# Kernel optimization log

Measured on AMD Instinct MI355X. Metric: run time of the kernel, lower is better.

The kernel has to match this reference:

```python
import jax, jax.numpy as jnp
import numpy as np

B, T_ENC, T_DEC = 8, 1024, 100
DMODEL, H, DK, DV, DFF = 512, 8, 64, 64, 2048
L_ENC, L_DEC = 2, 2
EPS = 1e-5
MASK_FILL = -1e10  # original code masked_fills the post-softmax probs with -1e10


def _ln(x, g, b):
    m = jnp.mean(x, -1, keepdims=True)
    v = jnp.mean(jnp.square(x - m), -1, keepdims=True)
    return (x - m) * jax.lax.rsqrt(v + EPS) * g + b


def _mha(Q, K, V, Wq, Wk, Wv, causal):
    Bz, Lq, _ = Q.shape
    Lk = K.shape[1]
    q = (Q @ Wq).reshape(Bz, Lq, H, DK).transpose(0, 2, 1, 3)  # b h q d
    k = (K @ Wk).reshape(Bz, Lk, H, DK).transpose(0, 2, 1, 3)
    v = (V @ Wv).reshape(Bz, Lk, H, DV).transpose(0, 2, 1, 3)
    scores = jnp.einsum('bhqd,bhkd->bhqk', q, k) * (1.0 / np.float32(np.sqrt(DK)))
    p = jax.nn.softmax(scores, axis=-1)
    if causal:
        # faithful to original: mask applied AFTER softmax, fill value -1e10
        mask = jnp.tril(jnp.ones((Lq, Lk), dtype=bool))
        p = jnp.where(mask[None, None], p, jnp.float32(MASK_FILL))
    o = jnp.einsum('bhqk,bhkd->bhqd', p, v)
    return o.transpose(0, 2, 1, 3).reshape(Bz, Lq, H * DV)


def setup_inputs() -> dict:
    key = jax.random.key(0)
    ks = iter(jax.random.split(key, 64))
    s = 0.02
    d = {
        'x': jax.random.normal(next(ks), (B, T_ENC, DMODEL), jnp.float32),
        'y': jax.random.normal(next(ks), (B, T_DEC, DMODEL), jnp.float32),
    }
    def w(shape):
        return jax.random.normal(next(ks), shape, jnp.float32) * s
    # encoder params, stacked over layers
    d['enc_Wq'] = w((L_ENC, DMODEL, DMODEL)); d['enc_Wk'] = w((L_ENC, DMODEL, H * DK))
    d['enc_Wv'] = w((L_ENC, DMODEL, H * DV))
    d['enc_ff_w1'] = w((L_ENC, DMODEL, DFF)); d['enc_ff_b1'] = jnp.zeros((L_ENC, DFF))
    d['enc_ff_w2'] = w((L_ENC, DFF, DMODEL)); d['enc_ff_b2'] = jnp.zeros((L_ENC, DMODEL))
    d['enc_ln1_g'] = jnp.ones((L_ENC, DMODEL)); d['enc_ln1_b'] = jnp.zeros((L_ENC, DMODEL))
    d['enc_ln2_g'] = jnp.ones((L_ENC, DMODEL)); d['enc_ln2_b'] = jnp.zeros((L_ENC, DMODEL))
    # decoder params
    d['dec_Wq1'] = w((L_DEC, DMODEL, DMODEL)); d['dec_Wk1'] = w((L_DEC, DMODEL, H * DK))
    d['dec_Wv1'] = w((L_DEC, DMODEL, H * DV))
    d['dec_Wq2'] = w((L_DEC, DMODEL, DMODEL)); d['dec_Wk2'] = w((L_DEC, DMODEL, H * DK))
    d['dec_Wv2'] = w((L_DEC, DMODEL, H * DV))
    d['dec_ff_w1'] = w((L_DEC, DMODEL, DFF)); d['dec_ff_b1'] = jnp.zeros((L_DEC, DFF))
    d['dec_ff_w2'] = w((L_DEC, DFF, DMODEL)); d['dec_ff_b2'] = jnp.zeros((L_DEC, DMODEL))
    d['dec_ln1_g'] = jnp.ones((L_DEC, DMODEL)); d['dec_ln1_b'] = jnp.zeros((L_DEC, DMODEL))
    d['dec_ln2_g'] = jnp.ones((L_DEC, DMODEL)); d['dec_ln2_b'] = jnp.zeros((L_DEC, DMODEL))
    d['dec_ln3_g'] = jnp.ones((L_DEC, DMODEL)); d['dec_ln3_b'] = jnp.zeros((L_DEC, DMODEL))
    return d


def reference(x, y,
              enc_Wq, enc_Wk, enc_Wv, enc_ff_w1, enc_ff_b1, enc_ff_w2, enc_ff_b2,
              enc_ln1_g, enc_ln1_b, enc_ln2_g, enc_ln2_b,
              dec_Wq1, dec_Wk1, dec_Wv1, dec_Wq2, dec_Wk2, dec_Wv2,
              dec_ff_w1, dec_ff_b1, dec_ff_w2, dec_ff_b2,
              dec_ln1_g, dec_ln1_b, dec_ln2_g, dec_ln2_b, dec_ln3_g, dec_ln3_b):
    # encoder stacks
    for i in range(L_ENC):
        att = _mha(x, x, x, enc_Wq[i], enc_Wk[i], enc_Wv[i], causal=False)
        x1 = _ln(x + att, enc_ln1_g[i], enc_ln1_b[i])
        ff = jax.nn.relu(x1 @ enc_ff_w1[i] + enc_ff_b1[i]) @ enc_ff_w2[i] + enc_ff_b2[i]
        x = _ln(x1 + ff, enc_ln2_g[i], enc_ln2_b[i])
    # decoder stacks
    for i in range(L_DEC):
        a1 = _mha(y, y, y, dec_Wq1[i], dec_Wk1[i], dec_Wv1[i], causal=True)
        y1 = _ln(y + a1, dec_ln1_g[i], dec_ln1_b[i])
        a2 = _mha(y1, x, x, dec_Wq2[i], dec_Wk2[i], dec_Wv2[i], causal=False)
        y2 = _ln(y1 + a2, dec_ln2_g[i], dec_ln2_b[i])
        ff = jax.nn.relu(y2 @ dec_ff_w1[i] + dec_ff_b1[i]) @ dec_ff_w2[i] + dec_ff_b2[i]
        y = _ln(y2 + ff, dec_ln3_g[i], dec_ln3_b[i])
    return y
```

## Files before the change

### kernel.cpp

```cpp
#include <hip/hip_runtime.h>
#include <cstddef>

typedef unsigned short u16;
typedef __attribute__((ext_vector_type(8))) short bf16x8;
typedef __attribute__((ext_vector_type(4))) float f32x4;

__device__ __forceinline__ u16 f2b(float f) {
    union { float f; unsigned u; } x; x.f = f;
    unsigned r = x.u + 0x7FFFu + ((x.u >> 16) & 1u);
    return (u16)(r >> 16);
}
__device__ __forceinline__ float b2f(u16 v) {
    union { unsigned u; float f; } x; x.u = ((unsigned)v) << 16;
    return x.f;
}

__device__ __forceinline__ void gload_lds16(const u16* g, u16* l) {
    __builtin_amdgcn_global_load_lds(
        (const __attribute__((address_space(1))) void*)g,
        (__attribute__((address_space(3))) void*)l, 16, 0, 0);
}

__global__ __launch_bounds__(256) void gemm_mfma_kernel(
    const u16* __restrict__ A, const u16* __restrict__ Bt,
    const float* __restrict__ bias,
    float* __restrict__ Cf, u16* __restrict__ Cb,
    int M, int K, int N, int relu)
{
    __shared__ __align__(16) u16 As[128 * 64];
    __shared__ __align__(16) u16 Bs[128 * 64];

    const int tid  = threadIdx.x;
    const int wave = tid >> 6;
    const int lane = tid & 63;
    const int m0 = blockIdx.y * 128;
    const int n0 = blockIdx.x * 128;

    const int wm = (wave & 1) * 64;
    const int wn = (wave >> 1) * 64;

    const int srow  = lane >> 3;
    const int skoff = (lane & 7) * 8;

    f32x4 acc[4][4];
#pragma unroll
    for (int i = 0; i < 4; ++i)
#pragma unroll
        for (int j = 0; j < 4; ++j)
            acc[i][j] = (f32x4){0.f, 0.f, 0.f, 0.f};

    const int fm = lane & 15;
    const int fq = (lane >> 4) * 8;

    for (int k0 = 0; k0 < K; k0 += 64) {
        __syncthreads();
        {
            const int r0 = wave * 32;
#pragma unroll
            for (int t = 0; t < 4; ++t) {
                int gr = m0 + r0 + t * 8 + srow; if (gr >= M) gr = M - 1;
                gload_lds16(A + (size_t)gr * K + k0 + skoff, &As[(r0 + t * 8) * 64]);
                gload_lds16(Bt + (size_t)(n0 + r0 + t * 8 + srow) * K + k0 + skoff,
                            &Bs[(r0 + t * 8) * 64]);
            }
        }
        __syncthreads();

#pragma unroll
        for (int kk = 0; kk < 64; kk += 32) {
            bf16x8 af[4], bfr[4];
#pragma unroll
            for (int t = 0; t < 4; ++t) {
                af[t]  = *(const bf16x8*)(&As[(wm + t * 16 + fm) * 64 + fq + kk]);
                bfr[t] = *(const bf16x8*)(&Bs[(wn + t * 16 + fm) * 64 + fq + kk]);
            }
#pragma unroll
            for (int i = 0; i < 4; ++i)
#pragma unroll
                for (int j = 0; j < 4; ++j)
                    acc[i][j] = __builtin_amdgcn_mfma_f32_16x16x32_bf16(
                        af[i], bfr[j], acc[i][j], 0, 0, 0);
        }
    }

    const int col = lane & 15;
    const int rq  = (lane >> 4) * 4;
#pragma unroll
    for (int j = 0; j < 4; ++j) {
        const int gn = n0 + wn + j * 16 + col;
        const float bb = bias ? bias[gn] : 0.f;
#pragma unroll
        for (int i = 0; i < 4; ++i) {
            const int gmb = m0 + wm + i * 16 + rq;
#pragma unroll
            for (int r = 0; r < 4; ++r) {
                const int gm = gmb + r;
                if (gm < M) {
                    float v = acc[i][j][r] + bb;
                    if (relu) v = fmaxf(v, 0.f);
                    if (Cb) Cb[(size_t)gm * N + gn] = f2b(v);
                    else    Cf[(size_t)gm * N + gn] = v;
                }
            }
        }
    }
}

__global__ __launch_bounds__(256) void gemm64_kernel(
    const u16* __restrict__ A, const u16* __restrict__ Bt,
    const float* __restrict__ bias,
    float* __restrict__ Cf, u16* __restrict__ Cb,
    int M, int K, int N, int relu)
{
    __shared__ __align__(16) u16 As[64 * 64];
    __shared__ __align__(16) u16 Bs[64 * 64];

    const int tid  = threadIdx.x;
    const int wave = tid >> 6;
    const int lane = tid & 63;
    const int m0 = blockIdx.y * 64;
    const int n0 = blockIdx.x * 64;
    const int wm = (wave & 1) * 32;
    const int wn = (wave >> 1) * 32;

    const int srow  = lane >> 3;
    const int skoff = (lane & 7) * 8;

    f32x4 acc[2][2];
#pragma unroll
    for (int i = 0; i < 2; ++i)
#pragma unroll
        for (int j = 0; j < 2; ++j) acc[i][j] = (f32x4){0.f, 0.f, 0.f, 0.f};

    const int fm = lane & 15;
    const int fq = (lane >> 4) * 8;

    for (int k0 = 0; k0 < K; k0 += 64) {
        __syncthreads();
        {
#pragma unroll
            for (int t = 0; t < 2; ++t) {
                int gr = m0 + t * 32 + wave * 8 + srow; if (gr >= M) gr = M - 1;
                gload_lds16(A + (size_t)gr * K + k0 + skoff, &As[(t * 32 + wave * 8) * 64]);
                gload_lds16(Bt + (size_t)(n0 + t * 32 + wave * 8 + srow) * K + k0 + skoff,
                            &Bs[(t * 32 + wave * 8) * 64]);
            }
        }
        __syncthreads();

#pragma unroll
        for (int kk = 0; kk < 64; kk += 32) {
            bf16x8 af[2], bfr[2];
#pragma unroll
            for (int t = 0; t < 2; ++t) {
                af[t]  = *(const bf16x8*)(&As[(wm + t * 16 + fm) * 64 + fq + kk]);
                bfr[t] = *(const bf16x8*)(&Bs[(wn + t * 16 + fm) * 64 + fq + kk]);
            }
#pragma unroll
            for (int i = 0; i < 2; ++i)
#pragma unroll
                for (int j = 0; j < 2; ++j)
                    acc[i][j] = __builtin_amdgcn_mfma_f32_16x16x32_bf16(
                        af[i], bfr[j], acc[i][j], 0, 0, 0);
        }
    }

    const int col = lane & 15;
    const int rq  = (lane >> 4) * 4;
#pragma unroll
    for (int j = 0; j < 2; ++j) {
        const int gn = n0 + wn + j * 16 + col;
        const float bb = bias ? bias[gn] : 0.f;
#pragma unroll
        for (int i = 0; i < 2; ++i) {
            const int gmb = m0 + wm + i * 16 + rq;
#pragma unroll
            for (int r = 0; r < 4; ++r) {
                const int gm = gmb + r;
                if (gm < M) {
                    float v = acc[i][j][r] + bb;
                    if (relu) v = fmaxf(v, 0.f);
                    if (Cb) Cb[(size_t)gm * N + gn] = f2b(v);
                    else    Cf[(size_t)gm * N + gn] = v;
                }
            }
        }
    }
}

__global__ __launch_bounds__(256) void attn_mfma_kernel(
    const u16* __restrict__ Qp, const u16* __restrict__ Kp,
    const u16* __restrict__ Vp, u16* __restrict__ Op,
    int Lq, int Lk, int ldq, int ldkv, int ldo)
{
    const int q0 = blockIdx.x * 128;
    const int h  = blockIdx.y;
    const int b  = blockIdx.z;
    const int tid  = threadIdx.x;
    const int wave = tid >> 6;
    const int lane = tid & 63;
    const int c = lane & 15;
    const int g = lane >> 4;
    const float scale = 0.125f;

    __shared__ __align__(16) u16 Ks[128 * 72];
    __shared__ __align__(16) u16 Vs[64 * 144];
    __shared__ __align__(16) u16 Ps[128 * 144];

    bf16x8 aq[2][2];
#pragma unroll
    for (int half = 0; half < 2; ++half) {
        int qrow = q0 + wave * 32 + half * 16 + c;
        if (qrow > Lq - 1) qrow = Lq - 1;
        const u16* src = Qp + ((size_t)(b * Lq + qrow)) * ldq + h * 64 + g * 8;
        aq[half][0] = *(const bf16x8*)(src);
        aq[half][1] = *(const bf16x8*)(src + 32);
    }

    float den[2][4] = {};
    f32x4 o[2][4];
#pragma unroll
    for (int half = 0; half < 2; ++half)
#pragma unroll
        for (int j = 0; j < 4; ++j) o[half][j] = (f32x4){0.f, 0.f, 0.f, 0.f};

    const int srow = tid & 63;
    const int sseg = tid >> 6;

    for (int t = 0; t < (Lk >> 7); ++t) {
        const int k0 = t << 7;
        __syncthreads();
#pragma unroll
        for (int sub = 0; sub < 2; ++sub) {
            const int kr = k0 + sub * 64 + srow;
            const u16* kg = Kp + ((size_t)(b * Lk + kr)) * ldkv + h * 64;
            *(bf16x8*)(&Ks[(sub * 64 + srow) * 72 + sseg * 8])      = *(const bf16x8*)(kg + sseg * 8);
            *(bf16x8*)(&Ks[(sub * 64 + srow) * 72 + 32 + sseg * 8]) = *(const bf16x8*)(kg + 32 + sseg * 8);
            const u16* vg = Vp + ((size_t)(b * Lk + kr)) * ldkv + h * 64;
            bf16x8 v0 = *(const bf16x8*)(vg + sseg * 8);
            bf16x8 v1 = *(const bf16x8*)(vg + 32 + sseg * 8);
#pragma unroll
            for (int i = 0; i < 8; ++i) {
                Vs[(sseg * 8 + i) * 144 + sub * 64 + srow]      = (u16)v0[i];
                Vs[(32 + sseg * 8 + i) * 144 + sub * 64 + srow] = (u16)v1[i];
            }
        }
        __syncthreads();

#pragma unroll
        for (int half = 0; half < 2; ++half) {
            f32x4 s[8];
#pragma unroll
            for (int jn = 0; jn < 8; ++jn) s[jn] = (f32x4){0.f, 0.f, 0.f, 0.f};
#pragma unroll
            for (int jn = 0; jn < 8; ++jn) {
                bf16x8 b0 = *(const bf16x8*)(&Ks[(jn * 16 + c) * 72 + g * 8]);
                bf16x8 b1 = *(const bf16x8*)(&Ks[(jn * 16 + c) * 72 + 32 + g * 8]);
                s[jn] = __builtin_amdgcn_mfma_f32_16x16x32_bf16(aq[half][0], b0, s[jn], 0, 0, 0);
                s[jn] = __builtin_amdgcn_mfma_f32_16x16x32_bf16(aq[half][1], b1, s[jn], 0, 0, 0);
            }
#pragma unroll
            for (int jn = 0; jn < 8; ++jn)
#pragma unroll
                for (int r = 0; r < 4; ++r) {
                    const float p = __expf(s[jn][r] * scale);
                    den[half][r] += p;
                    Ps[(wave * 32 + half * 16 + g * 4 + r) * 144 + jn * 16 + c] = f2b(p);
                }
        }

        __asm__ volatile("s_waitcnt lgkmcnt(0)" ::: "memory");

#pragma unroll
        for (int half = 0; half < 2; ++half) {
            const int qr = (wave * 32 + half * 16 + c) * 144;
#pragma unroll
            for (int sub = 0; sub < 2; ++sub) {
                bf16x8 ap0 = *(const bf16x8*)(&Ps[qr + sub * 64 + g * 8]);
                bf16x8 ap1 = *(const bf16x8*)(&Ps[qr + sub * 64 + 32 + g * 8]);
#pragma unroll
                for (int jd = 0; jd < 4; ++jd) {
                    bf16x8 b0 = *(const bf16x8*)(&Vs[(jd * 16 + c) * 144 + sub * 64 + g * 8]);
                    bf16x8 b1 = *(const bf16x8*)(&Vs[(jd * 16 + c) * 144 + sub * 64 + 32 + g * 8]);
                    o[half][jd] = __builtin_amdgcn_mfma_f32_16x16x32_bf16(ap0, b0, o[half][jd], 0, 0, 0);
                    o[half][jd] = __builtin_amdgcn_mfma_f32_16x16x32_bf16(ap1, b1, o[half][jd], 0, 0, 0);
                }
            }
        }
    }

#pragma unroll
    for (int half = 0; half < 2; ++half)
#pragma unroll
        for (int r = 0; r < 4; ++r) {
#pragma unroll
            for (int msk = 1; msk < 16; msk <<= 1)
                den[half][r] += __shfl_xor(den[half][r], msk, 64);
        }

#pragma unroll
    for (int half = 0; half < 2; ++half)
#pragma unroll
        for (int r = 0; r < 4; ++r) {
            const int q = q0 + wave * 32 + half * 16 + g * 4 + r;
            if (q < Lq) {
                const float inv = 1.0f / den[half][r];
#pragma unroll
                for (int jd = 0; jd < 4; ++jd)
                    Op[((size_t)(b * Lq + q)) * ldo + h * 64 + jd * 16 + c] =
                        f2b(o[half][jd][r] * inv);
            }
        }
}

__global__ __launch_bounds__(256) void attn_causal_kernel(
    const u16* __restrict__ Qp, const u16* __restrict__ Kp,
    const u16* __restrict__ Vp, const float* __restrict__ SuffV,
    u16* __restrict__ Op,
    int Lq, int Lk, int ldq, int ldkv, int ldo)
{
    const int q0 = blockIdx.x * 128;
    const int h  = blockIdx.y;
    const int b  = blockIdx.z;
    const int tid  = threadIdx.x;
    const int wave = tid >> 6;
    const int lane = tid & 63;
    const int c = lane & 15;
    const int g = lane >> 4;
    const float scale = 0.125f;

    __shared__ __align__(16) u16 Ks[64 * 72];
    __shared__ __align__(16) u16 Vs[64 * 72];
    __shared__ __align__(16) u16 Ps[128 * 72];

    bf16x8 aq[2][2];
#pragma unroll
    for (int half = 0; half < 2; ++half) {
        int qrow = q0 + wave * 32 + half * 16 + c;
        if (qrow > Lq - 1) qrow = Lq - 1;
        const u16* src = Qp + ((size_t)(b * Lq + qrow)) * ldq + h * 64 + g * 8;
        aq[half][0] = *(const bf16x8*)(src);
        aq[half][1] = *(const bf16x8*)(src + 32);
    }

    float den[2][4] = {};
    f32x4 o[2][4];
#pragma unroll
    for (int half = 0; half < 2; ++half)
#pragma unroll
        for (int j = 0; j < 4; ++j) o[half][j] = (f32x4){0.f, 0.f, 0.f, 0.f};

    const int srow = tid & 63;
    const int sseg = tid >> 6;
    const int ntiles = (Lk + 63) >> 6;

    for (int t = 0; t < ntiles; ++t) {
        const int k0 = t << 6;
        __syncthreads();
        {
            int kr = k0 + srow; if (kr > Lk - 1) kr = Lk - 1;
            const u16* kg = Kp + ((size_t)(b * Lk + kr)) * ldkv + h * 64;
            *(bf16x8*)(&Ks[srow * 72 + sseg * 8])      = *(const bf16x8*)(kg + sseg * 8);
            *(bf16x8*)(&Ks[srow * 72 + 32 + sseg * 8]) = *(const bf16x8*)(kg + 32 + sseg * 8);
            const u16* vg = Vp + ((size_t)(b * Lk + kr)) * ldkv + h * 64;
            bf16x8 v0 = *(const bf16x8*)(vg + sseg * 8);
            bf16x8 v1 = *(const bf16x8*)(vg + 32 + sseg * 8);
#pragma unroll
            for (int i = 0; i < 8; ++i) {
                Vs[(sseg * 8 + i) * 72 + srow]      = (u16)v0[i];
                Vs[(32 + sseg * 8 + i) * 72 + srow] = (u16)v1[i];
            }
        }
        __syncthreads();

#pragma unroll
        for (int half = 0; half < 2; ++half) {
            f32x4 s[4];
#pragma unroll
            for (int jn = 0; jn < 4; ++jn) s[jn] = (f32x4){0.f, 0.f, 0.f, 0.f};
#pragma unroll
            for (int jn = 0; jn < 4; ++jn) {
                bf16x8 b0 = *(const bf16x8*)(&Ks[(jn * 16 + c) * 72 + g * 8]);
                bf16x8 b1 = *(const bf16x8*)(&Ks[(jn * 16 + c) * 72 + 32 + g * 8]);
                s[jn] = __builtin_amdgcn_mfma_f32_16x16x32_bf16(aq[half][0], b0, s[jn], 0, 0, 0);
                s[jn] = __builtin_amdgcn_mfma_f32_16x16x32_bf16(aq[half][1], b1, s[jn], 0, 0, 0);
            }
#pragma unroll
            for (int jn = 0; jn < 4; ++jn)
#pragma unroll
                for (int r = 0; r < 4; ++r) {
                    const int kcol = k0 + jn * 16 + c;
                    const int qrow = q0 + wave * 32 + half * 16 + g * 4 + r;
                    const float e = __expf(s[jn][r] * scale);
                    const float ev = (kcol < Lk) ? e : 0.f;
                    den[half][r] += ev;
                    const float pv = (kcol <= qrow) ? ev : 0.f;
                    Ps[(wave * 32 + half * 16 + g * 4 + r) * 72 + jn * 16 + c] = f2b(pv);
                }
        }

        __asm__ volatile("s_waitcnt lgkmcnt(0)" ::: "memory");

#pragma unroll
        for (int half = 0; half < 2; ++half) {
            bf16x8 ap0 = *(const bf16x8*)(&Ps[(wave * 32 + half * 16 + c) * 72 + g * 8]);
            bf16x8 ap1 = *(const bf16x8*)(&Ps[(wave * 32 + half * 16 + c) * 72 + 32 + g * 8]);
#pragma unroll
            for (int jd = 0; jd < 4; ++jd) {
                bf16x8 b0 = *(const bf16x8*)(&Vs[(jd * 16 + c) * 72 + g * 8]);
                bf16x8 b1 = *(const bf16x8*)(&Vs[(jd * 16 + c) * 72 + 32 + g * 8]);
                o[half][jd] = __builtin_amdgcn_mfma_f32_16x16x32_bf16(ap0, b0, o[half][jd], 0, 0, 0);
                o[half][jd] = __builtin_amdgcn_mfma_f32_16x16x32_bf16(ap1, b1, o[half][jd], 0, 0, 0);
            }
        }
    }

#pragma unroll
    for (int half = 0; half < 2; ++half)
#pragma unroll
        for (int r = 0; r < 4; ++r) {
#pragma unroll
            for (int msk = 1; msk < 16; msk <<= 1)
                den[half][r] += __shfl_xor(den[half][r], msk, 64);
        }

#pragma unroll
    for (int half = 0; half < 2; ++half)
#pragma unroll
        for (int r = 0; r < 4; ++r) {
            const int q = q0 + wave * 32 + half * 16 + g * 4 + r;
            if (q < Lq) {
                const float inv = 1.0f / den[half][r];
                const float* sv = SuffV + ((size_t)(b * Lq + q)) * 512 + h * 64;
#pragma unroll
                for (int jd = 0; jd < 4; ++jd)
                    Op[((size_t)(b * Lq + q)) * ldo + h * 64 + jd * 16 + c] =
                        f2b(o[half][jd][r] * inv - 1.0e10f * sv[jd * 16 + c]);
            }
        }
}

__global__ __launch_bounds__(64) void suffv_kernel(
    const u16* __restrict__ Vp, float* __restrict__ SuffV, int Lq, int ldv)
{
    const int b = blockIdx.x;
    const int h = blockIdx.y;
    const int d = threadIdx.x;
    float acc = 0.f;
    for (int q = Lq - 1; q >= 0; --q) {
        SuffV[((size_t)(b * Lq + q)) * 512 + h * 64 + d] = acc;
        acc += b2f(Vp[((size_t)(b * Lq + q)) * ldv + h * 64 + d]);
    }
}

__global__ __launch_bounds__(256) void attn_split_kernel(
    const u16* __restrict__ Qp, const u16* __restrict__ Kp,
    const u16* __restrict__ Vp, float* __restrict__ Opart,
    float* __restrict__ Dpart,
    int Lq, int Lk, int ldq, int ldkv, int nsplit)
{
    const int q0 = blockIdx.x * 64;
    const int h  = blockIdx.y;
    const int b  = blockIdx.z / nsplit;
    const int sp = blockIdx.z % nsplit;
    const int tid  = threadIdx.x;
    const int wave = tid >> 6;
    const int lane = tid & 63;
    const int c = lane & 15;
    const int g = lane >> 4;
    const float scale = 0.125f;
    const int rowsTot = gridDim.z / nsplit * Lq;

    __shared__ __align__(16) u16 Ks[64 * 72];
    __shared__ __align__(16) u16 Vs[64 * 72];
    __shared__ __align__(16) u16 Ps[64 * 72];

    bf16x8 aq[2];
    {
        int qrow = q0 + wave * 16 + c;
        if (qrow > Lq - 1) qrow = Lq - 1;
        const u16* src = Qp + ((size_t)(b * Lq + qrow)) * ldq + h * 64 + g * 8;
        aq[0] = *(const bf16x8*)(src);
        aq[1] = *(const bf16x8*)(src + 32);
    }

    float den[4] = {0.f, 0.f, 0.f, 0.f};
    f32x4 o[4];
#pragma unroll
    for (int j = 0; j < 4; ++j) o[j] = (f32x4){0.f, 0.f, 0.f, 0.f};

    const int srow = tid & 63;
    const int sseg = tid >> 6;
    const int ntile = (Lk >> 6) / nsplit;

    for (int t = sp * ntile; t < (sp + 1) * ntile; ++t) {
        const int k0 = t << 6;
        __syncthreads();
        {
            const u16* kg = Kp + ((size_t)(b * Lk + k0 + srow)) * ldkv + h * 64;
            *(bf16x8*)(&Ks[srow * 72 + sseg * 8])      = *(const bf16x8*)(kg + sseg * 8);
            *(bf16x8*)(&Ks[srow * 72 + 32 + sseg * 8]) = *(const bf16x8*)(kg + 32 + sseg * 8);
            const u16* vg = Vp + ((size_t)(b * Lk + k0 + srow)) * ldkv + h * 64;
            bf16x8 v0 = *(const bf16x8*)(vg + sseg * 8);
            bf16x8 v1 = *(const bf16x8*)(vg + 32 + sseg * 8);
#pragma unroll
            for (int i = 0; i < 8; ++i) {
                Vs[(sseg * 8 + i) * 72 + srow]      = (u16)v0[i];
                Vs[(32 + sseg * 8 + i) * 72 + srow] = (u16)v1[i];
            }
        }
        __syncthreads();

        f32x4 s[4];
#pragma unroll
        for (int jn = 0; jn < 4; ++jn) s[jn] = (f32x4){0.f, 0.f, 0.f, 0.f};
#pragma unroll
        for (int jn = 0; jn < 4; ++jn) {
            bf16x8 b0 = *(const bf16x8*)(&Ks[(jn * 16 + c) * 72 + g * 8]);
            bf16x8 b1 = *(const bf16x8*)(&Ks[(jn * 16 + c) * 72 + 32 + g * 8]);
            s[jn] = __builtin_amdgcn_mfma_f32_16x16x32_bf16(aq[0], b0, s[jn], 0, 0, 0);
            s[jn] = __builtin_amdgcn_mfma_f32_16x16x32_bf16(aq[1], b1, s[jn], 0, 0, 0);
        }
#pragma unroll
        for (int jn = 0; jn < 4; ++jn)
#pragma unroll
            for (int r = 0; r < 4; ++r) {
                const float p = __expf(s[jn][r] * scale);
                den[r] += p;
                Ps[(wave * 16 + g * 4 + r) * 72 + jn * 16 + c] = f2b(p);
            }

        __asm__ volatile("s_waitcnt lgkmcnt(0)" ::: "memory");

        bf16x8 ap0 = *(const bf16x8*)(&Ps[(wave * 16 + c) * 72 + g * 8]);
        bf16x8 ap1 = *(const bf16x8*)(&Ps[(wave * 16 + c) * 72 + 32 + g * 8]);
#pragma unroll
        for (int jd = 0; jd < 4; ++jd) {
            bf16x8 b0 = *(const bf16x8*)(&Vs[(jd * 16 + c) * 72 + g * 8]);
            bf16x8 b1 = *(const bf16x8*)(&Vs[(jd * 16 + c) * 72 + 32 + g * 8]);
            o[jd] = __builtin_amdgcn_mfma_f32_16x16x32_bf16(ap0, b0, o[jd], 0, 0, 0);
            o[jd] = __builtin_amdgcn_mfma_f32_16x16x32_bf16(ap1, b1, o[jd], 0, 0, 0);
        }
    }

#pragma unroll
    for (int r = 0; r < 4; ++r) {
#pragma unroll
        for (int msk = 1; msk < 16; msk <<= 1)
            den[r] += __shfl_xor(den[r], msk, 64);
    }

#pragma unroll
    for (int r = 0; r < 4; ++r) {
        const int q = q0 + wave * 16 + g * 4 + r;
        if (q < Lq) {
            const size_t prow = (size_t)sp * rowsTot + b * Lq + q;
#pragma unroll
            for (int jd = 0; jd < 4; ++jd)
                Opart[prow * 512 + h * 64 + jd * 16 + c] = o[jd][r];
            if (c == 0) Dpart[prow * 8 + h] = den[r];
        }
    }
}

__global__ __launch_bounds__(256) void combine_ln_kernel(
    const float* __restrict__ Opart, const float* __restrict__ Dpart,
    int nsplit, int nrows,
    const float* __restrict__ R,
    const float* __restrict__ g, const float* __restrict__ beta,
    float* __restrict__ O, u16* __restrict__ Ob)
{
    const int row = blockIdx.x * 4 + (threadIdx.x >> 6);
    const int lane = threadIdx.x & 63;
    if (row >= nrows) return;
    const size_t base = (size_t)row * 512 + lane * 8;
    const int h = lane >> 3;

    float sd = 0.f;
    float v[8] = {};
    for (int s = 0; s < nsplit; ++s) {
        sd += Dpart[((size_t)s * nrows + row) * 8 + h];
        const float* op = Opart + ((size_t)s * nrows + row) * 512 + lane * 8;
        float4 a = *(const float4*)(op);
        float4 b = *(const float4*)(op + 4);
        v[0] += a.x; v[1] += a.y; v[2] += a.z; v[3] += a.w;
        v[4] += b.x; v[5] += b.y; v[6] += b.z; v[7] += b.w;
    }
    const float invd = 1.0f / sd;
    {
        float4 a = *(const float4*)(R + base);
        float4 b = *(const float4*)(R + base + 4);
        v[0] = v[0] * invd + a.x; v[1] = v[1] * invd + a.y;
        v[2] = v[2] * invd + a.z; v[3] = v[3] * invd + a.w;
        v[4] = v[4] * invd + b.x; v[5] = v[5] * invd + b.y;
        v[6] = v[6] * invd + b.z; v[7] = v[7] * invd + b.w;
    }

    float sum = 0.f;
#pragma unroll
    for (int i = 0; i < 8; ++i) sum += v[i];
#pragma unroll
    for (int msk = 1; msk < 64; msk <<= 1) sum += __shfl_xor(sum, msk, 64);
    const float mean = sum * (1.0f / 512.0f);

    float var = 0.f;
#pragma unroll
    for (int i = 0; i < 8; ++i) { v[i] -= mean; var += v[i] * v[i]; }
#pragma unroll
    for (int msk = 1; msk < 64; msk <<= 1) var += __shfl_xor(var, msk, 64);
    const float rstd = rsqrtf(var * (1.0f / 512.0f) + 1e-5f);

    float o[8];
#pragma unroll
    for (int i = 0; i < 8; ++i)
        o[i] = v[i] * rstd * g[lane * 8 + i] + beta[lane * 8 + i];

    *(float4*)(O + base)     = make_float4(o[0], o[1], o[2], o[3]);
    *(float4*)(O + base + 4) = make_float4(o[4], o[5], o[6], o[7]);
    if (Ob) {
        bf16x8 ob;
#pragma unroll
        for (int i = 0; i < 8; ++i) ob[i] = (short)f2b(o[i]);
        *(bf16x8*)(Ob + base) = ob;
    }
}

struct WT9 { const float* src[9]; unsigned dst[9]; unsigned os[9]; };
struct WT4 { const float* src[4]; unsigned dst[4]; int K[4]; int N[4]; };

__device__ __forceinline__ void wtrans_tile(
    const float* Wl, u16* Wtl, int K, int N, int k0, int n0, int tid)
{
    __shared__ float t[32][33];
    const int tr = tid >> 3;
    const int tc = (tid & 7) * 4;
    float4 v = *(const float4*)(Wl + (size_t)(k0 + tr) * N + n0 + tc);
    t[tr][tc] = v.x; t[tr][tc + 1] = v.y; t[tr][tc + 2] = v.z; t[tr][tc + 3] = v.w;
    __syncthreads();
    ushort4 o;
    o.x = f2b(t[tc + 0][tr]); o.y = f2b(t[tc + 1][tr]);
    o.z = f2b(t[tc + 2][tr]); o.w = f2b(t[tc + 3][tr]);
    *(ushort4*)(Wtl + (size_t)(n0 + tr) * K + k0 + tc) = o;
}

__global__ __launch_bounds__(256) void wtrans9_kernel(WT9 d, u16* __restrict__ WB)
{
    const int w = blockIdx.z >> 1;
    const int layer = blockIdx.z & 1;
    const float* Wl = d.src[w] + (size_t)layer * 512 * 512;
    u16* Wtl = WB + d.dst[w] + (size_t)layer * d.os[w];
    wtrans_tile(Wl, Wtl, 512, 512, blockIdx.y * 32, blockIdx.x * 32, threadIdx.x);
}

__global__ __launch_bounds__(256) void wtrans4_kernel(WT4 d, u16* __restrict__ WB)
{
    const int w = blockIdx.z >> 1;
    const int layer = blockIdx.z & 1;
    const int K = d.K[w], N = d.N[w];
    const int k0 = blockIdx.y * 32, n0 = blockIdx.x * 32;
    if (k0 >= K || n0 >= N) return;
    const float* Wl = d.src[w] + (size_t)layer * K * N;
    u16* Wtl = WB + d.dst[w] + (size_t)layer * 1048576;
    wtrans_tile(Wl, Wtl, K, N, k0, n0, threadIdx.x);
}

__global__ __launch_bounds__(256) void conv2_kernel(
    const float* __restrict__ X0, u16* __restrict__ Y0, int n0,
    const float* __restrict__ X1, u16* __restrict__ Y1, int n1)
{
    int i = (blockIdx.x * 256 + threadIdx.x) * 8;
    const float* X; u16* Y;
    if (i < n0) { X = X0 + i; Y = Y0 + i; }
    else if (i < n0 + n1) { X = X1 + (i - n0); Y = Y1 + (i - n0); }
    else return;
    float4 a = *(const float4*)(X);
    float4 b = *(const float4*)(X + 4);
    ushort4 o0, o1;
    o0.x = f2b(a.x); o0.y = f2b(a.y); o0.z = f2b(a.z); o0.w = f2b(a.w);
    o1.x = f2b(b.x); o1.y = f2b(b.y); o1.z = f2b(b.z); o1.w = f2b(b.w);
    *(ushort4*)(Y) = o0;
    *(ushort4*)(Y + 4) = o1;
}

__global__ __launch_bounds__(256) void ln_kernel(
    const float* __restrict__ Xf, const u16* __restrict__ Xb,
    const float* __restrict__ R,
    const float* __restrict__ g, const float* __restrict__ beta,
    float* __restrict__ O, u16* __restrict__ Ob, int nrows)
{
    const int row = blockIdx.x * 4 + (threadIdx.x >> 6);
    const int lane = threadIdx.x & 63;
    if (row >= nrows) return;
    const size_t base = (size_t)row * 512 + lane * 8;

    float v[8];
    if (Xf) {
        float4 a = *(const float4*)(Xf + base);
        float4 b = *(const float4*)(Xf + base + 4);
        v[0] = a.x; v[1] = a.y; v[2] = a.z; v[3] = a.w;
        v[4] = b.x; v[5] = b.y; v[6] = b.z; v[7] = b.w;
    } else {
        bf16x8 xb = *(const bf16x8*)(Xb + base);
#pragma unroll
        for (int i = 0; i < 8; ++i) v[i] = b2f((u16)xb[i]);
    }
    {
        float4 a = *(const float4*)(R + base);
        float4 b = *(const float4*)(R + base + 4);
        v[0] += a.x; v[1] += a.y; v[2] += a.z; v[3] += a.w;
        v[4] += b.x; v[5] += b.y; v[6] += b.z; v[7] += b.w;
    }

    float sum = 0.f;
#pragma unroll
    for (int i = 0; i < 8; ++i) sum += v[i];
#pragma unroll
    for (int msk = 1; msk < 64; msk <<= 1) sum += __shfl_xor(sum, msk, 64);
    const float mean = sum * (1.0f / 512.0f);

    float var = 0.f;
#pragma unroll
    for (int i = 0; i < 8; ++i) { v[i] -= mean; var += v[i] * v[i]; }
#pragma unroll
    for (int msk = 1; msk < 64; msk <<= 1) var += __shfl_xor(var, msk, 64);
    const float rstd = rsqrtf(var * (1.0f / 512.0f) + 1e-5f);

    float o[8];
#pragma unroll
    for (int i = 0; i < 8; ++i)
        o[i] = v[i] * rstd * g[lane * 8 + i] + beta[lane * 8 + i];

    *(float4*)(O + base)     = make_float4(o[0], o[1], o[2], o[3]);
    *(float4*)(O + base + 4) = make_float4(o[4], o[5], o[6], o[7]);
    if (Ob) {
        bf16x8 ob;
#pragma unroll
        for (int i = 0; i < 8; ++i) ob[i] = (short)f2b(o[i]);
        *(bf16x8*)(Ob + base) = ob;
    }
}

extern "C" void kernel_launch(void* const* d_in, const int* in_sizes, int n_in,
                              void* d_out, int out_size, void* d_ws, size_t ws_size,
                              hipStream_t stream)
{
    const int B = 8, T_ENC = 1024, T_DEC = 100, DM = 512, DFF = 2048;
    const int ME = B * T_ENC;
    const int MD = B * T_DEC;
    const int L = 2;
    const int NSPLIT = 4;

    int idx = 0;
    const float* x0    = (const float*)d_in[idx++];
    const float* y0    = (const float*)d_in[idx++];
    const float* eWq   = (const float*)d_in[idx++];
    const float* eWk   = (const float*)d_in[idx++];
    const float* eWv   = (const float*)d_in[idx++];
    const float* eW1   = (const float*)d_in[idx++];
    const float* eB1   = (const float*)d_in[idx++];
    const float* eW2   = (const float*)d_in[idx++];
    const float* eB2   = (const float*)d_in[idx++];
    const float* eLn1g = (const float*)d_in[idx++];
    const float* eLn1b = (const float*)d_in[idx++];
    const float* eLn2g = (const float*)d_in[idx++];
    const float* eLn2b = (const float*)d_in[idx++];
    const float* dWq1  = (const float*)d_in[idx++];
    const float* dWk1  = (const float*)d_in[idx++];
    const float* dWv1  = (const float*)d_in[idx++];
    const float* dWq2  = (const float*)d_in[idx++];
    const float* dWk2  = (const float*)d_in[idx++];
    const float* dWv2  = (const float*)d_in[idx++];
    const float* dW1   = (const float*)d_in[idx++];
    const float* dB1   = (const float*)d_in[idx++];
    const float* dW2   = (const float*)d_in[idx++];
    const float* dB2   = (const float*)d_in[idx++];
    const float* dLn1g = (const float*)d_in[idx++];
    const float* dLn1b = (const float*)d_in[idx++];
    const float* dLn2g = (const float*)d_in[idx++];
    const float* dLn2b = (const float*)d_in[idx++];
    const float* dLn3g = (const float*)d_in[idx++];
    const float* dLn3b = (const float*)d_in[idx++];

    float* ws = (float*)d_ws;
    u16* OV    = (u16*)ws;
    u16* QKVb  = OV;
    u16* H1b   = OV;
    u16* CKVb  = OV;
    u16* AFb    = (u16*)(ws + 8388608);
    float* Dpart = ws + 8388608;
    float* X1   = ws + 10485760;
    float* XOUT = ws + 14680064;
    float* SuffV = ws + 18874368;
    float* Opart = ws + 18874368;
    float* DA    = ws + 20103168;
    float* Y1   = ws + 20512768;
    float* Y2   = ws + 20922368;
    float* YOUT = ws + 21331968;
    u16* ub  = (u16*)(ws + 21741568);
    u16* XBc = ub;
    u16* YB  = ub + 4194304;
    u16* Y1b = ub + 4603904;
    u16* Y2b = ub + 5013504;
    u16* DQb = ub + 5423104;
    u16* DAb = ub + 5832704;
    u16* DHb = ub + 6242304;
    u16* DQKVb = DHb;
    u16* WB  = ub + 7880704;

    const unsigned eQKVT = 0, eW1T = 1572864, eW2T = 3670016,
                   dQKV1T = 5767168, dWq2T = 7340032, dKV2T = 7864320,
                   dW1T = 8912896, dW2T = 11010048;

    auto gemm = [&](const u16* A, const u16* Bt, const float* bias, float* Cf, u16* Cb,
                    int M, int K, int N, int relu) {
        dim3 grid(N / 128, (M + 127) / 128);
        hipLaunchKernelGGL(gemm_mfma_kernel, grid, dim3(256), 0, stream,
                           A, Bt, bias, Cf, Cb, M, K, N, relu);
    };
    auto gemm64 = [&](const u16* A, const u16* Bt, const float* bias, float* Cf, u16* Cb,
                      int M, int K, int N, int relu) {
        dim3 grid(N / 64, (M + 63) / 64);
        hipLaunchKernelGGL(gemm64_kernel, grid, dim3(256), 0, stream,
                           A, Bt, bias, Cf, Cb, M, K, N, relu);
    };
    auto ln = [&](const float* Xf, const u16* Xb, const float* R, const float* g,
                  const float* bta, float* O, u16* Ob, int rows) {
        hipLaunchKernelGGL(ln_kernel, dim3((rows + 3) / 4), dim3(256), 0, stream,
                           Xf, Xb, R, g, bta, O, Ob, rows);
    };

    {
        WT9 w9;
        const float* s9[9] = {eWq, eWk, eWv, dWq1, dWk1, dWv1, dWq2, dWk2, dWv2};
        const unsigned d9[9] = {eQKVT, eQKVT + 262144, eQKVT + 524288,
                                dQKV1T, dQKV1T + 262144, dQKV1T + 524288,
                                dWq2T, dKV2T, dKV2T + 262144};
        const unsigned o9[9] = {786432, 786432, 786432, 786432, 786432, 786432,
                                262144, 524288, 524288};
        for (int i = 0; i < 9; ++i) { w9.src[i] = s9[i]; w9.dst[i] = d9[i]; w9.os[i] = o9[i]; }
        hipLaunchKernelGGL(wtrans9_kernel, dim3(16, 16, 18), dim3(256), 0, stream, w9, WB);

        WT4 w4;
        const float* s4[4] = {eW1, eW2, dW1, dW2};
        const unsigned d4[4] = {eW1T, eW2T, dW1T, dW2T};
        const int K4[4] = {512, 2048, 512, 2048};
        const int N4[4] = {2048, 512, 2048, 512};
        for (int i = 0; i < 4; ++i) { w4.src[i] = s4[i]; w4.dst[i] = d4[i]; w4.K[i] = K4[i]; w4.N[i] = N4[i]; }
        hipLaunchKernelGGL(wtrans4_kernel, dim3(64, 64, 8), dim3(256), 0, stream, w4, WB);

        const int n0 = ME * DM, n1 = MD * DM;
        hipLaunchKernelGGL(conv2_kernel, dim3((n0 + n1) / 8 / 256), dim3(256), 0, stream,
                           x0, XBc, n0, y0, YB, n1);
    }

    const int BS = DM;
    const int B1S = DFF;

    const float* xin = x0;
    for (int i = 0; i < L; ++i) {
        gemm(XBc, WB + eQKVT + (size_t)i * 786432, nullptr, nullptr, QKVb, ME, DM, 1536, 0);
        {
            dim3 grid(T_ENC / 128, 8, B);
            hipLaunchKernelGGL(attn_mfma_kernel, grid, dim3(256), 0, stream,
                               QKVb, QKVb + 512, QKVb + 1024, AFb,
                               T_ENC, T_ENC, 1536, 1536, 512);
        }
        ln(nullptr, AFb, xin, eLn1g + i * BS, eLn1b + i * BS, X1, XBc, ME);
        gemm(XBc, WB + eW1T + (size_t)i * 1048576, eB1 + i * B1S, nullptr, H1b, ME, DM, DFF, 1);
        gemm(H1b, WB + eW2T + (size_t)i * 1048576, eB2 + i * BS, nullptr, AFb, ME, DFF, DM, 0);
        ln(nullptr, AFb, X1, eLn2g + i * BS, eLn2b + i * BS, XOUT, XBc, ME);
        xin = XOUT;
    }

    gemm(XBc, WB + dKV2T, nullptr, nullptr, CKVb, ME, DM, 2048, 0);

    const float* yin = y0;
    for (int i = 0; i < L; ++i) {
        gemm64(YB, WB + dQKV1T + (size_t)i * 786432, nullptr, nullptr, DQKVb, MD, DM, 1536, 0);
        hipLaunchKernelGGL(suffv_kernel, dim3(B, 8), dim3(64), 0, stream,
                           DQKVb + 1024, SuffV, T_DEC, 1536);
        {
            dim3 grid((T_DEC + 127) / 128, 8, B);
            hipLaunchKernelGGL(attn_causal_kernel, grid, dim3(256), 0, stream,
                               DQKVb, DQKVb + 512, DQKVb + 1024, SuffV, DAb,
                               T_DEC, T_DEC, 1536, 1536, 512);
        }
        ln(nullptr, DAb, yin, dLn1g + i * BS, dLn1b + i * BS, Y1, Y1b, MD);
        gemm64(Y1b, WB + dWq2T + (size_t)i * 262144, nullptr, nullptr, DQb, MD, DM, DM, 0);
        {
            dim3 grid((T_DEC + 63) / 64, 8, B * NSPLIT);
            hipLaunchKernelGGL(attn_split_kernel, grid, dim3(256), 0, stream,
                               DQb, CKVb + (size_t)i * 1024, CKVb + (size_t)i * 1024 + 512,
                               Opart, Dpart, T_DEC, T_ENC, 512, 2048, NSPLIT);
            hipLaunchKernelGGL(combine_ln_kernel, dim3((MD + 3) / 4), dim3(256), 0, stream,
                               Opart, Dpart, NSPLIT, MD,
                               Y1, dLn2g + i * BS, dLn2b + i * BS, Y2, Y2b);
        }
        gemm64(Y2b, WB + dW1T + (size_t)i * 1048576, dB1 + i * B1S, nullptr, DHb, MD, DM, DFF, 1);
        gemm64(DHb, WB + dW2T + (size_t)i * 1048576, dB2 + i * BS, DA, nullptr, MD, DFF, DM, 0);
        float* yout = (i == L - 1) ? (float*)d_out : YOUT;
        ln(DA, nullptr, Y2, dLn3g + i * BS, dLn3b + i * BS, yout,
           (i == L - 1) ? nullptr : YB, MD);
        yin = yout;
    }
}
```

Measured before the change: 863.1 us.

## Double-buffer LDS tiles in MFMA GEMM kernels with K-step of 32

Both GEMM kernels now keep two LDS buffers with a K-tile of 32 instead of a single 64-wide buffer. The next tile's global-to-LDS load is issued before the current tile's MFMAs run, using manual vmcnt/lgkmcnt waits and raw barriers in place of __syncthreads. The goal is to hide global load latency behind compute. In exchange there are twice as many loop iterations and barriers per K, and correctness depends on the hand-tuned waitcnt counts.

```diff
diff --git a/kernel.cpp b/kernel.cpp
--- a/kernel.cpp
+++ b/kernel.cpp
@@ -27,8 +27,8 @@
     float* __restrict__ Cf, u16* __restrict__ Cb,
     int M, int K, int N, int relu)
 {
-    __shared__ __align__(16) u16 As[128 * 64];
-    __shared__ __align__(16) u16 Bs[128 * 64];
+    __shared__ __align__(16) u16 As[2][128 * 32];
+    __shared__ __align__(16) u16 Bs[2][128 * 32];
 
     const int tid  = threadIdx.x;
     const int wave = tid >> 6;
@@ -39,8 +39,16 @@
     const int wm = (wave & 1) * 64;
     const int wn = (wave >> 1) * 64;
 
-    const int srow  = lane >> 3;
-    const int skoff = (lane & 7) * 8;
+    const int srow  = lane >> 2;
+    const int skoff = (lane & 3) * 8;
+
+    const int r0 = wave * 32;
+    int gr0 = m0 + r0 + srow;       if (gr0 >= M) gr0 = M - 1;
+    int gr1 = m0 + r0 + 16 + srow;  if (gr1 >= M) gr1 = M - 1;
+    const u16* a0 = A + (size_t)gr0 * K + skoff;
+    const u16* a1 = A + (size_t)gr1 * K + skoff;
+    const u16* b0p = Bt + (size_t)(n0 + r0 + srow) * K + skoff;
+    const u16* b1p = Bt + (size_t)(n0 + r0 + 16 + srow) * K + skoff;
 
     f32x4 acc[4][4];
 #pragma unroll
@@ -50,37 +58,44 @@
             acc[i][j] = (f32x4){0.f, 0.f, 0.f, 0.f};
 
     const int fm = lane & 15;
-    const int fq = (lane >> 4) * 8;
-
-    for (int k0 = 0; k0 < K; k0 += 64) {
-        __syncthreads();
-        {
-            const int r0 = wave * 32;
-#pragma unroll
-            for (int t = 0; t < 4; ++t) {
-                int gr = m0 + r0 + t * 8 + srow; if (gr >= M) gr = M - 1;
-                gload_lds16(A + (size_t)gr * K + k0 + skoff, &As[(r0 + t * 8) * 64]);
-                gload_lds16(Bt + (size_t)(n0 + r0 + t * 8 + srow) * K + k0 + skoff,
-                            &Bs[(r0 + t * 8) * 64]);
-            }
-        }
-        __syncthreads();
-
-#pragma unroll
-        for (int kk = 0; kk < 64; kk += 32) {
-            bf16x8 af[4], bfr[4];
-#pragma unroll
-            for (int t = 0; t < 4; ++t) {
-                af[t]  = *(const bf16x8*)(&As[(wm + t * 16 + fm) * 64 + fq + kk]);
-                bfr[t] = *(const bf16x8*)(&Bs[(wn + t * 16 + fm) * 64 + fq + kk]);
-            }
-#pragma unroll
-            for (int i = 0; i < 4; ++i)
-#pragma unroll
-                for (int j = 0; j < 4; ++j)
-                    acc[i][j] = __builtin_amdgcn_mfma_f32_16x16x32_bf16(
-                        af[i], bfr[j], acc[i][j], 0, 0, 0);
-        }
+    const int fk = (lane >> 4) * 8;
+
+    const int NK = K >> 5;
+
+    gload_lds16(a0, &As[0][(r0) * 32]);
+    gload_lds16(a1, &As[0][(r0 + 16) * 32]);
+    gload_lds16(b0p, &Bs[0][(r0) * 32]);
+    gload_lds16(b1p, &Bs[0][(r0 + 16) * 32]);
+
+    for (int t = 0; t < NK; ++t) {
+        const int cur = t & 1;
+        __asm__ volatile("s_waitcnt lgkmcnt(0)" ::: "memory");
+        __builtin_amdgcn_s_barrier();
+        if (t + 1 < NK) {
+            const int nxt = (t + 1) & 1;
+            const int ko = (t + 1) << 5;
+            gload_lds16(a0 + ko, &As[nxt][(r0) * 32]);
+            gload_lds16(a1 + ko, &As[nxt][(r0 + 16) * 32]);
+            gload_lds16(b0p + ko, &Bs[nxt][(r0) * 32]);
+            gload_lds16(b1p + ko, &Bs[nxt][(r0 + 16) * 32]);
+            __asm__ volatile("s_waitcnt vmcnt(4)" ::: "memory");
+        } else {
+            __asm__ volatile("s_waitcnt vmcnt(0)" ::: "memory");
+        }
+        __builtin_amdgcn_s_barrier();
+
+        bf16x8 af[4], bfr[4];
+#pragma unroll
+        for (int u = 0; u < 4; ++u) {
+            af[u]  = *(const bf16x8*)(&As[cur][(wm + u * 16 + fm) * 32 + fk]);
+            bfr[u] = *(const bf16x8*)(&Bs[cur][(wn + u * 16 + fm) * 32 + fk]);
+        }
+#pragma unroll
+        for (int i = 0; i < 4; ++i)
+#pragma unroll
+            for (int j = 0; j < 4; ++j)
+                acc[i][j] = __builtin_amdgcn_mfma_f32_16x16x32_bf16(
+                    af[i], bfr[j], acc[i][j], 0, 0, 0);
     }
 
     const int col = lane & 15;
@@ -112,8 +127,8 @@
     float* __restrict__ Cf, u16* __restrict__ Cb,
     int M, int K, int N, int relu)
 {
-    __shared__ __align__(16) u16 As[64 * 64];
-    __shared__ __align__(16) u16 Bs[64 * 64];
+    __shared__ __align__(16) u16 As[2][64 * 32];
+    __shared__ __align__(16) u16 Bs[2][64 * 32];
 
     const int tid  = threadIdx.x;
     const int wave = tid >> 6;
@@ -123,8 +138,12 @@
     const int wm = (wave & 1) * 32;
     const int wn = (wave >> 1) * 32;
 
-    const int srow  = lane >> 3;
-    const int skoff = (lane & 7) * 8;
+    const int srow  = lane >> 2;
+    const int skoff = (lane & 3) * 8;
+
+    int gr = m0 + wave * 16 + srow; if (gr >= M) gr = M - 1;
+    const u16* ap = A + (size_t)gr * K + skoff;
+    const u16* bp = Bt + (size_t)(n0 + wave * 16 + srow) * K + skoff;
 
     f32x4 acc[2][2];
 #pragma unroll
@@ -133,36 +152,40 @@
         for (int j = 0; j < 2; ++j) acc[i][j] = (f32x4){0.f, 0.f, 0.f, 0.f};
 
     const int fm = lane & 15;
-    const int fq = (lane >> 4) * 8;
-
-    for (int k0 = 0; k0 < K; k0 += 64) {
-        __syncthreads();
-        {
-#pragma unroll
-            for (int t = 0; t < 2; ++t) {
-                int gr = m0 + t * 32 + wave * 8 + srow; if (gr >= M) gr = M - 1;
-                gload_lds16(A + (size_t)gr * K + k0 + skoff, &As[(t * 32 + wave * 8) * 64]);
-                gload_lds16(Bt + (size_t)(n0 + t * 32 + wave * 8 + srow) * K + k0 + skoff,
-                            &Bs[(t * 32 + wave * 8) * 64]);
-            }
-        }
-        __syncthreads();
-
-#pragma unroll
-        for (int kk = 0; kk < 64; kk += 32) {
-            bf16x8 af[2], bfr[2];
-#pragma unroll
-            for (int t = 0; t < 2; ++t) {
-                af[t]  = *(const bf16x8*)(&As[(wm + t * 16 + fm) * 64 + fq + kk]);
-                bfr[t] = *(const bf16x8*)(&Bs[(wn + t * 16 + fm) * 64 + fq + kk]);
-            }
-#pragma unroll
-            for (int i = 0; i < 2; ++i)
-#pragma unroll
-                for (int j = 0; j < 2; ++j)
-                    acc[i][j] = __builtin_amdgcn_mfma_f32_16x16x32_bf16(
-                        af[i], bfr[j], acc[i][j], 0, 0, 0);
-        }
+    const int fk = (lane >> 4) * 8;
+
+    const int NK = K >> 5;
+
+    gload_lds16(ap, &As[0][(wave * 16) * 32]);
+    gload_lds16(bp, &Bs[0][(wave * 16) * 32]);
+
+    for (int t = 0; t < NK; ++t) {
+        const int cur = t & 1;
+        __asm__ volatile("s_waitcnt lgkmcnt(0)" ::: "memory");
+        __builtin_amdgcn_s_barrier();
+        if (t + 1 < NK) {
+            const int nxt = (t + 1) & 1;
+            const int ko = (t + 1) << 5;
+            gload_lds16(ap + ko, &As[nxt][(wave * 16) * 32]);
+            gload_lds16(bp + ko, &Bs[nxt][(wave * 16) * 32]);
+            __asm__ volatile("s_waitcnt vmcnt(2)" ::: "memory");
+        } else {
+            __asm__ volatile("s_waitcnt vmcnt(0)" ::: "memory");
+        }
+        __builtin_amdgcn_s_barrier();
+
+        bf16x8 af[2], bfr[2];
+#pragma unroll
+        for (int u = 0; u < 2; ++u) {
+            af[u]  = *(const bf16x8*)(&As[cur][(wm + u * 16 + fm) * 32 + fk]);
+            bfr[u] = *(const bf16x8*)(&Bs[cur][(wn + u * 16 + fm) * 32 + fk]);
+        }
+#pragma unroll
+        for (int i = 0; i < 2; ++i)
+#pragma unroll
+            for (int j = 0; j < 2; ++j)
+                acc[i][j] = __builtin_amdgcn_mfma_f32_16x16x32_bf16(
+                    af[i], bfr[j], acc[i][j], 0, 0, 0);
     }
 
     const int col = lane & 15;
```

After: 830.7 us. 3.8% less time.
